# Performance work log

Hardware: AMD Instinct MI355X
Metric: run time of the kernel (lower is better)

Reference implementation:

```python
import jax, jax.numpy as jnp
import numpy as np
import math

B, S, H = 2, 2048, 2048
NH, LD = 16, 512
HD = H // NH


def setup_inputs() -> dict:
    key = jax.random.key(0)
    ks = jax.random.split(key, 9)
    sc = 0.02
    return {
        "x": jax.random.normal(ks[0], (B, S, H), dtype=jnp.float32),
        "wq": jax.random.normal(ks[1], (H, H), dtype=jnp.float32) * sc,
        "bq": jnp.zeros((H,), dtype=jnp.float32),
        "wk_lat": jax.random.normal(ks[2], (H, LD), dtype=jnp.float32) * sc,
        "wv_lat": jax.random.normal(ks[3], (H, LD), dtype=jnp.float32) * sc,
        "wk": jax.random.normal(ks[4], (LD, H), dtype=jnp.float32) * sc,
        "wv": jax.random.normal(ks[5], (LD, H), dtype=jnp.float32) * sc,
        "wo": jax.random.normal(ks[6], (H, H), dtype=jnp.float32) * sc,
        "bo": jnp.zeros((H,), dtype=jnp.float32),
    }


def reference(x, wq, bq, wk_lat, wv_lat, wk, wv, wo, bo):
    b, s, _ = x.shape
    # projections
    q = (x @ wq + bq).reshape(b, s, NH, HD).transpose(0, 2, 1, 3)  # [B,NH,S,HD]
    k_lat = x @ wk_lat  # [B,S,LD]
    v_lat = x @ wv_lat
    k = (k_lat @ wk).reshape(b, s, NH, HD).transpose(0, 2, 1, 3)
    v = (v_lat @ wv).reshape(b, s, NH, HD).transpose(0, 2, 1, 3)
    # causal attention
    scores = jnp.einsum('bhqd,bhkd->bhqk', q, k) / math.sqrt(HD)
    mask = jnp.tril(jnp.ones((s, s), dtype=bool))  # True = keep
    scores = jnp.where(mask, scores, -jnp.inf)
    weights = jax.nn.softmax(scores, axis=-1)
    out = jnp.einsum('bhqk,bhkd->bhqd', weights, v)
    out = out.transpose(0, 2, 1, 3).reshape(b, s, H)
    return out @ wo + bo
```

## Files before the change

### kernel.cpp

```cpp
#include <hip/hip_runtime.h>
#include <hip/hip_bf16.h>
#include <type_traits>

#define PB   2
#define PS   2048
#define PH   2048
#define PNH  16
#define PLD  512
#define PHD  128
#define PM   (PB * PS)
#define PNCAT 3072
#define ATT_SCALE 0.08838834764831845f
#define ATT_MOFF 4.0f

typedef __attribute__((ext_vector_type(8))) short bf16x8;
typedef __attribute__((ext_vector_type(4))) float f32x4;

__device__ __forceinline__ unsigned short f2bf(float f) {
    unsigned int u = __float_as_uint(f);
    u += 0x7FFFu + ((u >> 16) & 1u);
    return (unsigned short)(u >> 16);
}

__device__ __forceinline__ void gl_lds16(const unsigned short* g, unsigned short* l) {
    __builtin_amdgcn_global_load_lds(
        (const __attribute__((address_space(1))) unsigned int*)g,
        (__attribute__((address_space(3))) unsigned int*)l, 16, 0, 0);
}

#define VMCNT(n)   asm volatile("s_waitcnt vmcnt(" #n ")" ::: "memory")
#define LGKM0()    asm volatile("s_waitcnt lgkmcnt(0)" ::: "memory")
#define MEMFENCE() asm volatile("" ::: "memory")

using btru = std::integral_constant<bool, true>;
using bfls = std::integral_constant<bool, false>;
using ib0  = std::integral_constant<int, 0>;
using ib1  = std::integral_constant<int, 1>;

__global__ __launch_bounds__(256) void cast_f32_bf16_kernel(
    const float* __restrict__ in, unsigned short* __restrict__ out, int n)
{
    int i = (blockIdx.x * 256 + threadIdx.x) * 4;
    if (i >= n) return;
    float4 f = *(const float4*)(in + i);
    unsigned int a = (unsigned int)f2bf(f.x) | ((unsigned int)f2bf(f.y) << 16);
    unsigned int b = (unsigned int)f2bf(f.z) | ((unsigned int)f2bf(f.w) << 16);
    *(uint2*)(out + i) = make_uint2(a, b);
}

__global__ __launch_bounds__(256) void transpose_cast_kernel(
    const float* __restrict__ in, unsigned short* __restrict__ out, int R, int C)
{
    __shared__ float tile[32][33];
    int tx = threadIdx.x, ty = threadIdx.y;
    int r0 = blockIdx.y * 32, c0 = blockIdx.x * 32;
#pragma unroll
    for (int i = 0; i < 32; i += 8)
        tile[ty + i][tx] = in[(size_t)(r0 + ty + i) * C + (c0 + tx)];
    __syncthreads();
#pragma unroll
    for (int i = 0; i < 32; i += 8)
        out[(size_t)(c0 + ty + i) * R + (r0 + tx)] = f2bf(tile[tx][ty + i]);
}

template<int BM, int EPI, bool HAS_BIAS>
__global__ __launch_bounds__(512, 2) void gemm8p_kernel(
    const unsigned short* __restrict__ A, int lda,
    const unsigned short* __restrict__ BT,
    const float* __restrict__ bias, int nbias,
    void* __restrict__ Cout, int ldc, int K)
{
    constexpr int MR  = BM / 32;
    constexpr int MH  = MR / 2;
    constexpr int ASZ = BM * 64;
    __shared__ __align__(16) unsigned short lds[2 * ASZ + 32768];

    const int tid  = threadIdx.x;
    const int wave = tid >> 6, lane = tid & 63;
    const int wm = wave >> 2, wn = wave & 3;
    const int quad = lane >> 4, l15 = lane & 15;
    const int sw = l15 & 7;

    const int gx  = gridDim.x;
    const int nwg = gx * gridDim.y;
    int wg = blockIdx.y * gx + blockIdx.x;
    if (!(nwg & 7)) wg = (wg & 7) * (nwg >> 3) + (wg >> 3);
    const int bm = (wg / gx) * BM, bn = (wg % gx) * 256;

    const int nt = K >> 6;

    const int srow = tid >> 3;
    const int scol = ((tid & 7) ^ (srow & 7)) << 3;
    const unsigned short* Ag = A  + (size_t)(bm + srow) * lda + scol;
    const unsigned short* Bg = BT + (size_t)(bn + srow) * K   + scol;
    unsigned short* const ldsA = &lds[wave * 512];
    unsigned short* const ldsB = &lds[2 * ASZ + wave * 512];

    auto stA64 = [&](int kt, int sub, int b) {
        gl_lds16(Ag + (size_t)(sub * 64) * lda + kt * 64, ldsA + b * ASZ + sub * 4096);
    };
    auto stB64 = [&](int kt, int sub, int b) {
        gl_lds16(Bg + (size_t)(sub * 64) * K + kt * 64, ldsB + b * 16384 + sub * 4096);
    };
    auto stAlo = [&](int kt, int b) { stA64(kt, 0, b); if constexpr (BM == 256) stA64(kt, 1, b); };
    auto stAhi = [&](int kt, int b) { if constexpr (BM == 256) { stA64(kt, 2, b); stA64(kt, 3, b); }
                                      else stA64(kt, 1, b); };
    auto stBlo = [&](int kt, int b) { stB64(kt, 0, b); stB64(kt, 1, b); };
    auto stBhi = [&](int kt, int b) { stB64(kt, 2, b); stB64(kt, 3, b); };

    auto ldA = [&](int b, int m, int ks) -> bf16x8 {
        int ra = m * 32 + wm * 16 + l15;
        return *(const bf16x8*)&lds[b * ASZ + ra * 64 + (((ks * 4 + quad) ^ sw) << 3)];
    };
    auto ldB = [&](int b, int j, int ks) -> bf16x8 {
        int rb = j * 64 + wn * 16 + l15;
        return *(const bf16x8*)&lds[2 * ASZ + b * 16384 + rb * 64 + (((ks * 4 + quad) ^ sw) << 3)];
    };

    f32x4 acc[MR][4] = {};

    auto tile = [&](auto bc, auto s1c, auto s2c, int t) {
        constexpr int  b  = decltype(bc)::value;
        constexpr int  nb = b ^ 1;
        constexpr bool s1 = decltype(s1c)::value;
        constexpr bool s2 = decltype(s2c)::value;
        bf16x8 af[MH][2], bfr[2][2];

#pragma unroll
        for (int m = 0; m < MH; ++m)
#pragma unroll
            for (int ks = 0; ks < 2; ++ks) af[m][ks] = ldA(b, m, ks);
#pragma unroll
        for (int j = 0; j < 2; ++j)
#pragma unroll
            for (int ks = 0; ks < 2; ++ks) bfr[j][ks] = ldB(b, j, ks);
        if constexpr (s1) stBlo(t + 1, nb);
        __builtin_amdgcn_s_barrier();
        LGKM0();
        __builtin_amdgcn_sched_barrier(0);
        __builtin_amdgcn_s_setprio(1);
#pragma unroll
        for (int m = 0; m < MH; ++m)
#pragma unroll
            for (int j = 0; j < 2; ++j)
#pragma unroll
                for (int ks = 0; ks < 2; ++ks)
                    acc[m][j] = __builtin_amdgcn_mfma_f32_16x16x32_bf16(af[m][ks], bfr[j][ks], acc[m][j], 0, 0, 0);
        __builtin_amdgcn_s_setprio(0);
        __builtin_amdgcn_s_barrier();

#pragma unroll
        for (int j = 0; j < 2; ++j)
#pragma unroll
            for (int ks = 0; ks < 2; ++ks) bfr[j][ks] = ldB(b, 2 + j, ks);
        __builtin_amdgcn_s_barrier();
        LGKM0();
        __builtin_amdgcn_sched_barrier(0);
        __builtin_amdgcn_s_setprio(1);
#pragma unroll
        for (int m = 0; m < MH; ++m)
#pragma unroll
            for (int j = 0; j < 2; ++j)
#pragma unroll
                for (int ks = 0; ks < 2; ++ks)
                    acc[m][2 + j] = __builtin_amdgcn_mfma_f32_16x16x32_bf16(af[m][ks], bfr[j][ks], acc[m][2 + j], 0, 0, 0);
        __builtin_amdgcn_s_setprio(0);
        __builtin_amdgcn_s_barrier();

#pragma unroll
        for (int m = 0; m < MH; ++m)
#pragma unroll
            for (int ks = 0; ks < 2; ++ks) af[m][ks] = ldA(b, MH + m, ks);
        if constexpr (s2) stAlo(t + 2, b);
        __builtin_amdgcn_s_barrier();
        LGKM0();
        __builtin_amdgcn_sched_barrier(0);
        __builtin_amdgcn_s_setprio(1);
#pragma unroll
        for (int m = 0; m < MH; ++m)
#pragma unroll
            for (int j = 0; j < 2; ++j)
#pragma unroll
                for (int ks = 0; ks < 2; ++ks)
                    acc[MH + m][2 + j] = __builtin_amdgcn_mfma_f32_16x16x32_bf16(af[m][ks], bfr[j][ks], acc[MH + m][2 + j], 0, 0, 0);
        __builtin_amdgcn_s_setprio(0);
        __builtin_amdgcn_s_barrier();

#pragma unroll
        for (int j = 0; j < 2; ++j)
#pragma unroll
            for (int ks = 0; ks < 2; ++ks) bfr[j][ks] = ldB(b, j, ks);
        if constexpr (s2) { stAhi(t + 2, b); stBhi(t + 2, b); }
        __builtin_amdgcn_s_barrier();
        LGKM0();
        __builtin_amdgcn_sched_barrier(0);
        __builtin_amdgcn_s_setprio(1);
#pragma unroll
        for (int m = 0; m < MH; ++m)
#pragma unroll
            for (int j = 0; j < 2; ++j)
#pragma unroll
                for (int ks = 0; ks < 2; ++ks)
                    acc[MH + m][j] = __builtin_amdgcn_mfma_f32_16x16x32_bf16(af[m][ks], bfr[j][ks], acc[MH + m][j], 0, 0, 0);
        __builtin_amdgcn_s_setprio(0);
        if constexpr (s2) { if constexpr (BM == 256) { VMCNT(6); } else { VMCNT(4); } }
        else              { VMCNT(0); }
        __builtin_amdgcn_s_barrier();
        MEMFENCE();
    };

    stAlo(0, 0); stAhi(0, 0); stBlo(0, 0); stBhi(0, 0);
    stAlo(1, 1); stAhi(1, 1); stBhi(1, 1);
    if constexpr (BM == 256) { VMCNT(6); } else { VMCNT(4); }
    __builtin_amdgcn_s_barrier();
    MEMFENCE();

    int t = 0;
    for (; t + 3 < nt; t += 2) {
        tile(ib0{}, btru{}, btru{}, t);
        tile(ib1{}, btru{}, btru{}, t + 1);
    }
    tile(ib0{}, btru{}, bfls{}, nt - 2);
    tile(ib1{}, bfls{}, bfls{}, nt - 1);

#pragma unroll
    for (int m = 0; m < MR; ++m)
#pragma unroll
        for (int j = 0; j < 4; ++j)
#pragma unroll
            for (int r = 0; r < 4; ++r) {
                int row = bm + m * 32 + wm * 16 + quad * 4 + r;
                int col = bn + j * 64 + wn * 16 + l15;
                float val = acc[m][j][r];
                if (HAS_BIAS && col < nbias) val += bias[col];
                if (EPI == 2) {
                    int bb = row >> 11, s = row & 2047, hh = col >> 7, d = col & 127;
                    size_t idx = ((size_t)((bb << 4) + hh) << 18) + ((size_t)(s >> 6) << 13)
                               + ((d >> 3) << 9) + ((s & 63) << 3) + (d & 7);
                    ((unsigned short*)Cout)[idx] = f2bf(val);
                } else if (EPI == 3) {
                    int bb = row >> 11, s = row & 2047, hh = col >> 7, d = col & 127;
                    size_t idx = ((size_t)((bb << 4) + hh) << 18) + ((size_t)(s >> 6) << 13)
                               + (((s >> 3) & 7) << 10) + (d << 3) + (s & 7);
                    ((unsigned short*)Cout)[idx] = f2bf(val);
                } else if (EPI == 1) {
                    ((float*)Cout)[(size_t)row * ldc + col] = val;
                } else {
                    ((unsigned short*)Cout)[(size_t)row * ldc + col] = f2bf(val);
                }
            }
}

__global__ __launch_bounds__(256) void flash_attn_mfma_kernel(
    const unsigned short* __restrict__ q,
    const unsigned short* __restrict__ kswz,
    const unsigned short* __restrict__ vswz,
    unsigned short* __restrict__ o)
{
    __shared__ __align__(16) unsigned short Kl[2][8192];
    __shared__ __align__(16) unsigned short Vl[8192];
    __shared__ __align__(16) unsigned short Ps[4][16][72];

    const int tid  = threadIdx.x;
    const int wave = tid >> 6;
    const int lane = tid & 63;
    const int quad = lane >> 4, l15 = lane & 15;

    const int bid = blockIdx.x;
    const int qt = 31 - (bid >> 5);
    const int bh = bid & 31;
    const int b  = bh >> 4, h = bh & 15;
    const int q0 = qt * 64;

    const unsigned short* qbase = q + (size_t)(b * PS + q0) * PNCAT + h * PHD;
    const unsigned short* kbase = kswz + ((size_t)bh << 18);
    const unsigned short* vbase = vswz + ((size_t)bh << 18);

    auto stageK = [&](int it, int buf) {
        const unsigned short* kt = kbase + ((size_t)it << 13);
#pragma unroll
        for (int j = 0; j < 4; ++j)
            gl_lds16(kt + (wave * 4 + j) * 512 + lane * 8, &Kl[buf][(wave * 4 + j) * 512]);
    };
    auto stageV = [&](int it) {
        const unsigned short* vt = vbase + ((size_t)it << 13);
#pragma unroll
        for (int j = 0; j < 4; ++j)
            gl_lds16(vt + (wave * 4 + j) * 512 + lane * 8, &Vl[(wave * 4 + j) * 512]);
    };

    bf16x8 aq[4];
#pragma unroll
    for (int kk = 0; kk < 4; ++kk)
        aq[kk] = *(const bf16x8*)(qbase + (size_t)(wave * 16 + l15) * PNCAT + kk * 32 + quad * 8);

    bf16x8 vones;
#pragma unroll
    for (int j = 0; j < 8; ++j) vones[j] = (short)0x3F80;

    f32x4 oacc[8] = {};
    f32x4 lacc = {};

    stageK(0, 0);

    for (int it = 0; it <= qt; ++it) {
        const int cur = it & 1;
        __syncthreads();
        stageV(it);
        if (it < qt) stageK(it + 1, cur ^ 1);

        f32x4 sacc[4] = {};
#pragma unroll
        for (int kk = 0; kk < 4; ++kk)
#pragma unroll
            for (int n = 0; n < 4; ++n) {
                bf16x8 bk = *(const bf16x8*)&Kl[cur][((kk * 4 + quad) * 64 + n * 16 + l15) * 8];
                sacc[n] = __builtin_amdgcn_mfma_f32_16x16x32_bf16(aq[kk], bk, sacc[n], 0, 0, 0);
            }

        const bool diag = (it == qt);
#pragma unroll
        for (int n = 0; n < 4; ++n)
#pragma unroll
            for (int r = 0; r < 4; ++r) {
                float p = __expf(fmaf(sacc[n][r], ATT_SCALE, -ATT_MOFF));
                if (diag && (n * 16 + l15 > wave * 16 + quad * 4 + r)) p = 0.0f;
                Ps[wave][quad * 4 + r][n * 16 + l15] = f2bf(p);
            }

        __syncthreads();

#pragma unroll
        for (int kk = 0; kk < 2; ++kk) {
            bf16x8 ap = *(const bf16x8*)&Ps[wave][l15][kk * 32 + quad * 8];
            lacc = __builtin_amdgcn_mfma_f32_16x16x32_bf16(ap, vones, lacc, 0, 0, 0);
#pragma unroll
            for (int n = 0; n < 8; ++n) {
                bf16x8 bv = *(const bf16x8*)&Vl[((kk * 4 + quad) * 128 + n * 16 + l15) * 8];
                oacc[n] = __builtin_amdgcn_mfma_f32_16x16x32_bf16(ap, bv, oacc[n], 0, 0, 0);
            }
        }
    }

    float inv[4];
#pragma unroll
    for (int r = 0; r < 4; ++r) inv[r] = 1.0f / lacc[r];
#pragma unroll
    for (int n = 0; n < 8; ++n)
#pragma unroll
        for (int r = 0; r < 4; ++r) {
            int row = q0 + wave * 16 + quad * 4 + r;
            int col = h * PHD + n * 16 + l15;
            o[(size_t)(b * PS + row) * PH + col] = f2bf(oacc[n][r] * inv[r]);
        }
}

extern "C" void kernel_launch(void* const* d_in, const int* in_sizes, int n_in,
                              void* d_out, int out_size, void* d_ws, size_t ws_size,
                              hipStream_t stream)
{
    const float* x      = (const float*)d_in[0];
    const float* wq     = (const float*)d_in[1];
    const float* bq     = (const float*)d_in[2];
    const float* wk_lat = (const float*)d_in[3];
    const float* wv_lat = (const float*)d_in[4];
    const float* wk     = (const float*)d_in[5];
    const float* wv     = (const float*)d_in[6];
    const float* wo     = (const float*)d_in[7];
    const float* bo     = (const float*)d_in[8];
    float* out = (float*)d_out;

    char* ws = (char*)d_ws;
    size_t off = 0;
    auto alloc = [&](size_t bytes) -> void* {
        void* p = ws + off;
        off += (bytes + 255) & ~(size_t)255;
        return p;
    };
    unsigned short* xb    = (unsigned short*)alloc((size_t)PM * PH * 2);
    unsigned short* wcatT = (unsigned short*)alloc((size_t)PNCAT * PH * 2);
    unsigned short* wkT   = (unsigned short*)alloc((size_t)PH * PLD * 2);
    unsigned short* wvT   = (unsigned short*)alloc((size_t)PH * PLD * 2);
    unsigned short* woT   = (unsigned short*)alloc((size_t)PH * PH * 2);
    unsigned short* cat   = (unsigned short*)alloc((size_t)PM * PNCAT * 2);
    unsigned short* kswz  = (unsigned short*)alloc((size_t)PM * PH * 2);
    unsigned short* attn  = (unsigned short*)alloc((size_t)PM * PH * 2);
    unsigned short* vswz  = xb;

    unsigned short* wqT    = wcatT;
    unsigned short* wkLatT = wcatT + (size_t)PH * PH;
    unsigned short* wvLatT = wcatT + (size_t)(PH + PLD) * PH;

    dim3 tb(32, 8);

    cast_f32_bf16_kernel<<<(PM * PH) / 4 / 256, 256, 0, stream>>>(x, xb, PM * PH);
    transpose_cast_kernel<<<dim3(PH / 32,  PH / 32),  tb, 0, stream>>>(wq,     wqT,    PH,  PH);
    transpose_cast_kernel<<<dim3(PLD / 32, PH / 32),  tb, 0, stream>>>(wk_lat, wkLatT, PH,  PLD);
    transpose_cast_kernel<<<dim3(PLD / 32, PH / 32),  tb, 0, stream>>>(wv_lat, wvLatT, PH,  PLD);
    transpose_cast_kernel<<<dim3(PH / 32,  PLD / 32), tb, 0, stream>>>(wk,     wkT,    PLD, PH);
    transpose_cast_kernel<<<dim3(PH / 32,  PLD / 32), tb, 0, stream>>>(wv,     wvT,    PLD, PH);
    transpose_cast_kernel<<<dim3(PH / 32,  PH / 32),  tb, 0, stream>>>(wo,     woT,    PH,  PH);

    gemm8p_kernel<256, 0, true><<<dim3(PNCAT / 256, PM / 256), 512, 0, stream>>>(
        xb, PH, wcatT, bq, PH, cat, PNCAT, PH);

    gemm8p_kernel<128, 2, false><<<dim3(PH / 256, PM / 128), 512, 0, stream>>>(
        cat + PH, PNCAT, wkT, nullptr, 0, kswz, 0, PLD);
    gemm8p_kernel<128, 3, false><<<dim3(PH / 256, PM / 128), 512, 0, stream>>>(
        cat + PH + PLD, PNCAT, wvT, nullptr, 0, vswz, 0, PLD);

    flash_attn_mfma_kernel<<<PB * PNH * (PS / 64), 256, 0, stream>>>(cat, kswz, vswz, attn);

    gemm8p_kernel<128, 1, true><<<dim3(PH / 256, PM / 128), 512, 0, stream>>>(
        attn, PH, woT, bo, PH, out, PH, PH);
}
```

Measured before the change: 342.4 us.

## Replace 4-phase barrier-interleaved GEMM pipeline with simple double-buffered prefetch

The GEMM main loop changes from a fine-grained 4-phase schedule, with barriers, lgkmcnt waits, setprio and prefetch two tiles ahead, to a simpler double buffer. Each iteration now issues the full next tile's global-to-LDS loads up front, runs all MFMAs without intermediate barriers, then waits on vmcnt(0) and one barrier. This cuts barrier and synchronisation overhead but gives up the deeper prefetch distance and the explicit interleaving of LDS reads with MFMA, so load latency may be exposed.

```diff
diff --git a/kernel.cpp b/kernel.cpp
--- a/kernel.cpp
+++ b/kernel.cpp
@@ -29,7 +29,6 @@
 }
 
 #define VMCNT(n)   asm volatile("s_waitcnt vmcnt(" #n ")" ::: "memory")
-#define LGKM0()    asm volatile("s_waitcnt lgkmcnt(0)" ::: "memory")
 #define MEMFENCE() asm volatile("" ::: "memory")
 
 using btru = std::integral_constant<bool, true>;
@@ -102,11 +101,12 @@
     auto stB64 = [&](int kt, int sub, int b) {
         gl_lds16(Bg + (size_t)(sub * 64) * K + kt * 64, ldsB + b * 16384 + sub * 4096);
     };
-    auto stAlo = [&](int kt, int b) { stA64(kt, 0, b); if constexpr (BM == 256) stA64(kt, 1, b); };
-    auto stAhi = [&](int kt, int b) { if constexpr (BM == 256) { stA64(kt, 2, b); stA64(kt, 3, b); }
-                                      else stA64(kt, 1, b); };
-    auto stBlo = [&](int kt, int b) { stB64(kt, 0, b); stB64(kt, 1, b); };
-    auto stBhi = [&](int kt, int b) { stB64(kt, 2, b); stB64(kt, 3, b); };
+    auto stTile = [&](int kt, int b) {
+        stA64(kt, 0, b);
+        if constexpr (BM == 256) { stA64(kt, 1, b); stA64(kt, 2, b); stA64(kt, 3, b); }
+        else stA64(kt, 1, b);
+        stB64(kt, 0, b); stB64(kt, 1, b); stB64(kt, 2, b); stB64(kt, 3, b);
+    };
 
     auto ldA = [&](int b, int m, int ks) -> bf16x8 {
         int ra = m * 32 + wm * 16 + l15;
@@ -119,109 +119,74 @@
 
     f32x4 acc[MR][4] = {};
 
-    auto tile = [&](auto bc, auto s1c, auto s2c, int t) {
-        constexpr int  b  = decltype(bc)::value;
-        constexpr int  nb = b ^ 1;
-        constexpr bool s1 = decltype(s1c)::value;
-        constexpr bool s2 = decltype(s2c)::value;
-        bf16x8 af[MH][2], bfr[2][2];
-
-#pragma unroll
-        for (int m = 0; m < MH; ++m)
-#pragma unroll
-            for (int ks = 0; ks < 2; ++ks) af[m][ks] = ldA(b, m, ks);
+    auto tileT = [&](auto pc, auto stc, int t) {
+        constexpr int  p  = decltype(pc)::value;
+        constexpr bool st = decltype(stc)::value;
+        if constexpr (st) stTile(t + 1, p ^ 1);
+
+        bf16x8 af[MH][2], blr[2][2], bhr[2][2];
+#pragma unroll
+        for (int m = 0; m < MH; ++m)
+#pragma unroll
+            for (int ks = 0; ks < 2; ++ks) af[m][ks] = ldA(p, m, ks);
 #pragma unroll
         for (int j = 0; j < 2; ++j)
 #pragma unroll
-            for (int ks = 0; ks < 2; ++ks) bfr[j][ks] = ldB(b, j, ks);
-        if constexpr (s1) stBlo(t + 1, nb);
-        __builtin_amdgcn_s_barrier();
-        LGKM0();
-        __builtin_amdgcn_sched_barrier(0);
-        __builtin_amdgcn_s_setprio(1);
+            for (int ks = 0; ks < 2; ++ks) blr[j][ks] = ldB(p, j, ks);
 #pragma unroll
         for (int m = 0; m < MH; ++m)
 #pragma unroll
             for (int j = 0; j < 2; ++j)
 #pragma unroll
                 for (int ks = 0; ks < 2; ++ks)
-                    acc[m][j] = __builtin_amdgcn_mfma_f32_16x16x32_bf16(af[m][ks], bfr[j][ks], acc[m][j], 0, 0, 0);
-        __builtin_amdgcn_s_setprio(0);
-        __builtin_amdgcn_s_barrier();
-
+                    acc[m][j] = __builtin_amdgcn_mfma_f32_16x16x32_bf16(af[m][ks], blr[j][ks], acc[m][j], 0, 0, 0);
 #pragma unroll
         for (int j = 0; j < 2; ++j)
 #pragma unroll
-            for (int ks = 0; ks < 2; ++ks) bfr[j][ks] = ldB(b, 2 + j, ks);
-        __builtin_amdgcn_s_barrier();
-        LGKM0();
-        __builtin_amdgcn_sched_barrier(0);
-        __builtin_amdgcn_s_setprio(1);
+            for (int ks = 0; ks < 2; ++ks) bhr[j][ks] = ldB(p, 2 + j, ks);
 #pragma unroll
         for (int m = 0; m < MH; ++m)
 #pragma unroll
             for (int j = 0; j < 2; ++j)
 #pragma unroll
                 for (int ks = 0; ks < 2; ++ks)
-                    acc[m][2 + j] = __builtin_amdgcn_mfma_f32_16x16x32_bf16(af[m][ks], bfr[j][ks], acc[m][2 + j], 0, 0, 0);
-        __builtin_amdgcn_s_setprio(0);
-        __builtin_amdgcn_s_barrier();
-
-#pragma unroll
-        for (int m = 0; m < MH; ++m)
-#pragma unroll
-            for (int ks = 0; ks < 2; ++ks) af[m][ks] = ldA(b, MH + m, ks);
-        if constexpr (s2) stAlo(t + 2, b);
-        __builtin_amdgcn_s_barrier();
-        LGKM0();
-        __builtin_amdgcn_sched_barrier(0);
-        __builtin_amdgcn_s_setprio(1);
+                    acc[m][2 + j] = __builtin_amdgcn_mfma_f32_16x16x32_bf16(af[m][ks], bhr[j][ks], acc[m][2 + j], 0, 0, 0);
+        MEMFENCE();
+#pragma unroll
+        for (int m = 0; m < MH; ++m)
+#pragma unroll
+            for (int ks = 0; ks < 2; ++ks) af[m][ks] = ldA(p, MH + m, ks);
 #pragma unroll
         for (int m = 0; m < MH; ++m)
 #pragma unroll
             for (int j = 0; j < 2; ++j)
 #pragma unroll
                 for (int ks = 0; ks < 2; ++ks)
-                    acc[MH + m][2 + j] = __builtin_amdgcn_mfma_f32_16x16x32_bf16(af[m][ks], bfr[j][ks], acc[MH + m][2 + j], 0, 0, 0);
-        __builtin_amdgcn_s_setprio(0);
-        __builtin_amdgcn_s_barrier();
-
-#pragma unroll
-        for (int j = 0; j < 2; ++j)
-#pragma unroll
-            for (int ks = 0; ks < 2; ++ks) bfr[j][ks] = ldB(b, j, ks);
-        if constexpr (s2) { stAhi(t + 2, b); stBhi(t + 2, b); }
-        __builtin_amdgcn_s_barrier();
-        LGKM0();
-        __builtin_amdgcn_sched_barrier(0);
-        __builtin_amdgcn_s_setprio(1);
+                    acc[MH + m][2 + j] = __builtin_amdgcn_mfma_f32_16x16x32_bf16(af[m][ks], bhr[j][ks], acc[MH + m][2 + j], 0, 0, 0);
 #pragma unroll
         for (int m = 0; m < MH; ++m)
 #pragma unroll
             for (int j = 0; j < 2; ++j)
 #pragma unroll
                 for (int ks = 0; ks < 2; ++ks)
-                    acc[MH + m][j] = __builtin_amdgcn_mfma_f32_16x16x32_bf16(af[m][ks], bfr[j][ks], acc[MH + m][j], 0, 0, 0);
-        __builtin_amdgcn_s_setprio(0);
-        if constexpr (s2) { if constexpr (BM == 256) { VMCNT(6); } else { VMCNT(4); } }
-        else              { VMCNT(0); }
+                    acc[MH + m][j] = __builtin_amdgcn_mfma_f32_16x16x32_bf16(af[m][ks], blr[j][ks], acc[MH + m][j], 0, 0, 0);
+        VMCNT(0);
         __builtin_amdgcn_s_barrier();
         MEMFENCE();
     };
 
-    stAlo(0, 0); stAhi(0, 0); stBlo(0, 0); stBhi(0, 0);
-    stAlo(1, 1); stAhi(1, 1); stBhi(1, 1);
-    if constexpr (BM == 256) { VMCNT(6); } else { VMCNT(4); }
+    stTile(0, 0);
+    VMCNT(0);
     __builtin_amdgcn_s_barrier();
     MEMFENCE();
 
     int t = 0;
-    for (; t + 3 < nt; t += 2) {
-        tile(ib0{}, btru{}, btru{}, t);
-        tile(ib1{}, btru{}, btru{}, t + 1);
+    for (; t + 2 < nt; t += 2) {
+        tileT(ib0{}, btru{}, t);
+        tileT(ib1{}, btru{}, t + 1);
     }
-    tile(ib0{}, btru{}, bfls{}, nt - 2);
-    tile(ib1{}, bfls{}, bfls{}, nt - 1);
+    tileT(ib0{}, btru{}, nt - 2);
+    tileT(ib1{}, bfls{}, nt - 1);
 
 #pragma unroll
     for (int m = 0; m < MR; ++m)
```

Measured after the change: 359.1 us. 1.05x slower.
